# Optimization experiments

Measured on AMD Instinct MI355X. Metric: run time of the kernel, lower is better.

## Reference

```python
import jax, jax.numpy as jnp
import numpy as np

B, S, D = 4, 4096, 1024
H, W = 16, 256
DH = D // H


def setup_inputs() -> dict:
    key = jax.random.key(0)
    ks = jax.random.split(key, 5)
    sc = 1.0 / np.sqrt(D)
    return {
        "x": jax.random.normal(ks[0], (B, S, D), jnp.float32),
        "Wq": jax.random.normal(ks[1], (D, D), jnp.float32) * sc,
        "bq": jnp.zeros((D,), jnp.float32),
        "Wk": jax.random.normal(ks[2], (D, D), jnp.float32) * sc,
        "bk": jnp.zeros((D,), jnp.float32),
        "Wv": jax.random.normal(ks[3], (D, D), jnp.float32) * sc,
        "bv": jnp.zeros((D,), jnp.float32),
        "Wo": jax.random.normal(ks[4], (D, D), jnp.float32) * sc,
        "bo": jnp.zeros((D,), jnp.float32),
    }


def reference(x, Wq, bq, Wk, bk, Wv, bv, Wo, bo):
    b, s, d = x.shape
    n = s // W  # seq divisible by window_size -> no padding

    def split_heads(t):
        # (b, s, d) -> (b, h, n, w, dh)
        return t.reshape(b, n, W, H, DH).transpose(0, 3, 1, 2, 4)

    q = split_heads(x @ Wq + bq)
    k = split_heads(x @ Wk + bk)
    v = split_heads(x @ Wv + bv)

    scores = jnp.einsum("bhnqd,bhnkd->bhnqk", q, k) / jnp.sqrt(
        jnp.asarray(DH, x.dtype)
    )
    causal = jnp.tril(jnp.ones((W, W), bool))  # per-block causal mask
    neg = jnp.finfo(scores.dtype).min
    scores = jnp.where(causal, scores, neg)
    weights = jax.nn.softmax(scores, axis=-1)
    out = jnp.einsum("bhnqk,bhnkd->bhnqd", weights, v)
    # (b, h, n, w, dh) -> (b, s, d)
    out = out.transpose(0, 2, 3, 1, 4).reshape(b, s, d)
    return out @ Wo + bo
```

## Files before the change

kernel.cpp:

```cpp
#include <hip/hip_runtime.h>
#include <hip/hip_bf16.h>


typedef __attribute__((ext_vector_type(4))) float f32x4;
typedef __attribute__((ext_vector_type(8))) short s16x8;
typedef __attribute__((ext_vector_type(4))) short s16x4;

__device__ __forceinline__ short f2bf(float f) {
  unsigned u = __float_as_uint(f);
  u += 0x7fffu + ((u >> 16) & 1u);
  return (short)(u >> 16);
}

__device__ __forceinline__ void gload_lds16(const void* g, void* l) {
  __builtin_amdgcn_global_load_lds((const __attribute__((address_space(1))) void*)g,
                                   (__attribute__((address_space(3))) void*)l,
                                   16, 0, 0);
}

__device__ __forceinline__ float rmax16(float v) {
  v = fmaxf(v, __shfl_xor(v, 1, 64));
  v = fmaxf(v, __shfl_xor(v, 2, 64));
  v = fmaxf(v, __shfl_xor(v, 4, 64));
  v = fmaxf(v, __shfl_xor(v, 8, 64));
  return v;
}
__device__ __forceinline__ float rsum16(float v) {
  v += __shfl_xor(v, 1, 64);
  v += __shfl_xor(v, 2, 64);
  v += __shfl_xor(v, 4, 64);
  v += __shfl_xor(v, 8, 64);
  return v;
}

__global__ void cvt_x(const float4* __restrict__ in, s16x4* __restrict__ out, int n4) {
  for (int i = blockIdx.x * 256 + threadIdx.x; i < n4; i += gridDim.x * 256) {
    float4 v = in[i];
    s16x4 o;
    o[0] = f2bf(v.x); o[1] = f2bf(v.y); o[2] = f2bf(v.z); o[3] = f2bf(v.w);
    out[i] = o;
  }
}

__global__ void cvt_wT(const float* __restrict__ W0, const float* __restrict__ W1,
                       const float* __restrict__ W2, const float* __restrict__ W3,
                       short* __restrict__ out) {
  __shared__ float tile[64][65];
  const float* W = (blockIdx.y == 0) ? W0 : (blockIdx.y == 1) ? W1 : (blockIdx.y == 2) ? W2 : W3;
  short* o = out + (size_t)blockIdx.y * (1024 * 1024);
  const int kt = (blockIdx.x >> 4) << 6, nt = (blockIdx.x & 15) << 6;
  const int tid = threadIdx.x;
#pragma unroll
  for (int i = 0; i < 16; ++i) {
    int lin = i * 256 + tid;
    int r = lin >> 6, c = lin & 63;
    tile[r][c] = W[(size_t)(kt + r) * 1024 + nt + c];
  }
  __syncthreads();
#pragma unroll
  for (int i = 0; i < 16; ++i) {
    int lin = i * 256 + tid;
    int r = lin >> 6, c = lin & 63;
    o[(size_t)(nt + r) * 1024 + kt + c] = f2bf(tile[c][r]);
  }
}

template <int NBN, int MODE>
__global__ __launch_bounds__(512, 2) void gemm8(const short* __restrict__ A,
                                                const short* __restrict__ BtBase,
                                                const float* __restrict__ b0,
                                                const float* __restrict__ b1,
                                                const float* __restrict__ b2,
                                                short* __restrict__ Qo,
                                                short* __restrict__ Ko,
                                                short* __restrict__ Vo,
                                                float* __restrict__ Oo) {
  __shared__ short As[2][16384];
  __shared__ short Bs[2][16384];
  const int tid = threadIdx.x;
  const int wid = tid >> 6, lane = tid & 63;
  const int fr = lane & 15, g = lane >> 4;
  const int wr = wid >> 2, wc = wid & 3;
  const int fswz = (fr & 7) << 4;
  const int d = blockIdx.x;
  const int xcd = d & 7, l = d >> 3;
  const int bm = xcd * 8 + l / NBN, bn = l % NBN;
  const int m0 = bm << 8, n0 = bn << 8;
  const int which = n0 >> 10;
  const char* Ab = (const char*)(A + (size_t)m0 * 1024);
  const char* Bb = (const char*)(BtBase + (size_t)which * 1048576 + (size_t)(n0 & 1023) * 1024);

  const int srow = tid >> 3;
  const int kb = ((tid & 7) << 4) ^ ((srow & 7) << 4);
  const char* aSrc = Ab + (size_t)srow * 2048 + kb;
  const char* bSrc = Bb + (size_t)srow * 2048 + kb;
  const int ldsOff = wid << 10;

#define STAGE2(srcp, dstp, i0, tt)                                            \
  do {                                                                        \
    gload_lds16((srcp) + (size_t)(i0) * 131072 + (size_t)(tt) * 128,          \
                (dstp) + (i0) * 8192 + ldsOff);                               \
    gload_lds16((srcp) + (size_t)((i0) + 1) * 131072 + (size_t)(tt) * 128,    \
                (dstp) + ((i0) + 1) * 8192 + ldsOff);                         \
  } while (0)

#define AFRAG(mi, ks) (*(const s16x8*)(Acur + ((((wr) << 7) + (mi) * 16 + fr) << 7) + \
                                       ((((ks) << 6) | (g << 4)) ^ fswz)))
#define BFRAG(ni, ks) (*(const s16x8*)(Bcur + ((((wc) << 6) + (ni) * 16 + fr) << 7) + \
                                       ((((ks) << 6) | (g << 4)) ^ fswz)))

#define PHASE_MID()                                       \
  __builtin_amdgcn_s_barrier();                           \
  asm volatile("s_waitcnt lgkmcnt(0)" ::: "memory");      \
  __builtin_amdgcn_sched_barrier(0);                      \
  __builtin_amdgcn_s_setprio(1)

#define PHASE_END()                                       \
  __builtin_amdgcn_s_setprio(0);                          \
  __builtin_amdgcn_s_barrier()

  f32x4 acc[8][4];
#pragma unroll
  for (int i = 0; i < 8; ++i)
#pragma unroll
    for (int j = 0; j < 4; ++j) acc[i][j] = (f32x4){0.f, 0.f, 0.f, 0.f};

  {
    char* A0 = (char*)&As[0][0];
    char* B0 = (char*)&Bs[0][0];
    STAGE2(aSrc, A0, 0, 0); STAGE2(aSrc, A0, 2, 0);
    STAGE2(bSrc, B0, 0, 0); STAGE2(bSrc, B0, 2, 0);
  }

#pragma unroll 2
  for (int t = 0; t < 16; ++t) {
    const int cur = t & 1;
    const int tn = t + 1;
    const bool pre = (t < 15);
    const char* Acur = (const char*)&As[cur][0];
    const char* Bcur = (const char*)&Bs[cur][0];
    char* Anxt = (char*)&As[cur ^ 1][0];
    char* Bnxt = (char*)&Bs[cur ^ 1][0];

    asm volatile("s_waitcnt vmcnt(0)" ::: "memory");
    __builtin_amdgcn_s_barrier();

    s16x8 aF[2][4], bF0[2][2], bF1[2][2];
#pragma unroll
    for (int ks = 0; ks < 2; ++ks) {
#pragma unroll
      for (int mi = 0; mi < 4; ++mi) aF[ks][mi] = AFRAG(mi, ks);
#pragma unroll
      for (int ni = 0; ni < 2; ++ni) bF0[ks][ni] = BFRAG(ni, ks);
    }
    if (pre) STAGE2(aSrc, Anxt, 0, tn);
    PHASE_MID();
#pragma unroll
    for (int ks = 0; ks < 2; ++ks)
#pragma unroll
      for (int mi = 0; mi < 4; ++mi)
#pragma unroll
        for (int ni = 0; ni < 2; ++ni)
          acc[mi][ni] = __builtin_amdgcn_mfma_f32_16x16x32_bf16(aF[ks][mi], bF0[ks][ni], acc[mi][ni], 0, 0, 0);
    PHASE_END();

#pragma unroll
    for (int ks = 0; ks < 2; ++ks)
#pragma unroll
      for (int ni = 0; ni < 2; ++ni) bF1[ks][ni] = BFRAG(2 + ni, ks);
    if (pre) STAGE2(aSrc, Anxt, 2, tn);
    PHASE_MID();
#pragma unroll
    for (int ks = 0; ks < 2; ++ks)
#pragma unroll
      for (int mi = 0; mi < 4; ++mi)
#pragma unroll
        for (int ni = 0; ni < 2; ++ni)
          acc[mi][2 + ni] = __builtin_amdgcn_mfma_f32_16x16x32_bf16(aF[ks][mi], bF1[ks][ni], acc[mi][2 + ni], 0, 0, 0);
    PHASE_END();

#pragma unroll
    for (int ks = 0; ks < 2; ++ks)
#pragma unroll
      for (int mi = 0; mi < 4; ++mi) aF[ks][mi] = AFRAG(4 + mi, ks);
    if (pre) STAGE2(bSrc, Bnxt, 0, tn);
    PHASE_MID();
#pragma unroll
    for (int ks = 0; ks < 2; ++ks)
#pragma unroll
      for (int mi = 0; mi < 4; ++mi)
#pragma unroll
        for (int ni = 0; ni < 2; ++ni)
          acc[4 + mi][2 + ni] = __builtin_amdgcn_mfma_f32_16x16x32_bf16(aF[ks][mi], bF1[ks][ni], acc[4 + mi][2 + ni], 0, 0, 0);
    PHASE_END();

    if (pre) STAGE2(bSrc, Bnxt, 2, tn);
    PHASE_MID();
#pragma unroll
    for (int ks = 0; ks < 2; ++ks)
#pragma unroll
      for (int mi = 0; mi < 4; ++mi)
#pragma unroll
        for (int ni = 0; ni < 2; ++ni)
          acc[4 + mi][ni] = __builtin_amdgcn_mfma_f32_16x16x32_bf16(aF[ks][mi], bF0[ks][ni], acc[4 + mi][ni], 0, 0, 0);
    PHASE_END();
  }
#undef STAGE2
#undef AFRAG
#undef BFRAG
#undef PHASE_MID
#undef PHASE_END

  const float* bb = (which == 0) ? b0 : (which == 1) ? b1 : b2;
  const int row0 = m0 + wr * 128 + (g << 2);
  const int col0 = n0 + wc * 64 + fr;
#pragma unroll
  for (int mi = 0; mi < 8; ++mi) {
#pragma unroll
    for (int ni = 0; ni < 4; ++ni) {
      const int c = col0 + ni * 16;
      const float bv = bb[c & 1023];
#pragma unroll
      for (int jj = 0; jj < 4; ++jj) {
        const int r = row0 + mi * 16 + jj;
        const float v = acc[mi][ni][jj] + bv;
        if (MODE == 2) {
          Oo[(size_t)r * 1024 + c] = v;
        } else {
          const int b = r >> 12, s = r & 4095;
          const int cl = c & 1023;
          const int h = cl >> 6, dh = cl & 63;
          short* ob = (which == 0) ? Qo : (which == 1) ? Ko : Vo;
          size_t addr;
          if (which < 2) addr = ((size_t)(b * 16 + h) * 4096 + s) * 64 + dh;
          else           addr = ((size_t)(b * 16 + h) * 64 + dh) * 4096 + s;
          ob[addr] = f2bf(v);
        }
      }
    }
  }
}

__global__ __launch_bounds__(256) void attn_kernel(const short* __restrict__ Qg,
                                                   const short* __restrict__ Kg,
                                                   const short* __restrict__ Vg,
                                                   short* __restrict__ AO) {
  constexpr int S = 4096;
  __shared__ short Pl[4][16][272];
  const int tid = threadIdx.x;
  const int w = tid >> 6, lane = tid & 63;
  const int fr = lane & 15, g = lane >> 4;
  const int idx = blockIdx.x;
  const int qq = idx & 3;
  const int nb = (idx >> 2) & 15, bh = idx >> 6;
  const int b = bh >> 4, h = bh & 15;
  const short* Qb = Qg + ((size_t)bh * S + nb * 256) * 64;
  const short* Kb = Kg + ((size_t)bh * S + nb * 256) * 64;
  const short* Vb = Vg + (size_t)bh * 64 * S + nb * 256;

  const int qrow = qq * 64 + w * 16;
  const int dmax = qq * 4 + w;
  const s16x8 aq0 = *(const s16x8*)&Qb[(qrow + fr) * 64 + (g << 3)];
  const s16x8 aq1 = *(const s16x8*)&Qb[(qrow + fr) * 64 + 32 + (g << 3)];
  f32x4 sc[16];
#pragma unroll
  for (int i = 0; i < 16; ++i) sc[i] = (f32x4){0.f, 0.f, 0.f, 0.f};
#pragma unroll
  for (int kt = 0; kt < 16; ++kt) {
    if (kt <= dmax) {
      const s16x8 kf0 = *(const s16x8*)&Kb[(kt * 16 + fr) * 64 + (g << 3)];
      const s16x8 kf1 = *(const s16x8*)&Kb[(kt * 16 + fr) * 64 + 32 + (g << 3)];
      sc[kt] = __builtin_amdgcn_mfma_f32_16x16x32_bf16(aq0, kf0, sc[kt], 0, 0, 0);
      sc[kt] = __builtin_amdgcn_mfma_f32_16x16x32_bf16(aq1, kf1, sc[kt], 0, 0, 0);
    }
  }
  float mrow[4] = {-3e38f, -3e38f, -3e38f, -3e38f};
#pragma unroll
  for (int kt = 0; kt < 16; ++kt) {
    if (kt <= dmax) {
#pragma unroll
      for (int jj = 0; jj < 4; ++jj) {
        float v = sc[kt][jj] * 0.125f;
        if (kt == dmax && fr > (g << 2) + jj) v = -3e38f;
        sc[kt][jj] = v;
        mrow[jj] = fmaxf(mrow[jj], v);
      }
    }
  }
#pragma unroll
  for (int jj = 0; jj < 4; ++jj) mrow[jj] = rmax16(mrow[jj]);
  float lsum[4] = {0.f, 0.f, 0.f, 0.f};
#pragma unroll
  for (int kt = 0; kt < 16; ++kt) {
    if (kt <= dmax) {
#pragma unroll
      for (int jj = 0; jj < 4; ++jj) {
        const float p = __expf(sc[kt][jj] - mrow[jj]);
        sc[kt][jj] = p;
        lsum[jj] += p;
      }
    }
  }
#pragma unroll
  for (int jj = 0; jj < 4; ++jj) lsum[jj] = rsum16(lsum[jj]);
#pragma unroll
  for (int kt = 0; kt < 16; ++kt) {
    if (kt <= dmax) {
#pragma unroll
      for (int jj = 0; jj < 4; ++jj)
        Pl[w][(g << 2) + jj][kt * 16 + fr] = f2bf(sc[kt][jj]);
    } else if (kt == dmax + 1 && ((dmax + 1) & 1)) {
#pragma unroll
      for (int jj = 0; jj < 4; ++jj) Pl[w][(g << 2) + jj][kt * 16 + fr] = 0;
    }
  }
  asm volatile("s_waitcnt lgkmcnt(0)" ::: "memory");
  f32x4 o[4];
#pragma unroll
  for (int di = 0; di < 4; ++di) o[di] = (f32x4){0.f, 0.f, 0.f, 0.f};
  const int nks2 = (dmax + 2) >> 1;
#pragma unroll
  for (int ks2 = 0; ks2 < 8; ++ks2) {
    if (ks2 < nks2) {
      const s16x8 pa = *(const s16x8*)&Pl[w][fr][ks2 * 32 + (g << 3)];
#pragma unroll
      for (int di = 0; di < 4; ++di) {
        const s16x8 vf = *(const s16x8*)&Vb[(size_t)(di * 16 + fr) * S + ks2 * 32 + (g << 3)];
        o[di] = __builtin_amdgcn_mfma_f32_16x16x32_bf16(pa, vf, o[di], 0, 0, 0);
      }
    }
  }
  float inv[4];
#pragma unroll
  for (int jj = 0; jj < 4; ++jj) inv[jj] = 1.f / lsum[jj];
  const int sg = nb * 256 + qrow + (g << 2);
#pragma unroll
  for (int di = 0; di < 4; ++di) {
#pragma unroll
    for (int jj = 0; jj < 4; ++jj) {
      AO[((size_t)b * S + sg + jj) * 1024 + h * 64 + di * 16 + fr] =
          f2bf(o[di][jj] * inv[jj]);
    }
  }
}

extern "C" void kernel_launch(void* const* d_in, const int* in_sizes, int n_in,
                              void* d_out, int out_size, void* d_ws, size_t ws_size,
                              hipStream_t stream) {
  const float* x  = (const float*)d_in[0];
  const float* Wq = (const float*)d_in[1];
  const float* bq = (const float*)d_in[2];
  const float* Wk = (const float*)d_in[3];
  const float* bk = (const float*)d_in[4];
  const float* Wv = (const float*)d_in[5];
  const float* bv = (const float*)d_in[6];
  const float* Wo = (const float*)d_in[7];
  const float* bo = (const float*)d_in[8];
  float* out = (float*)d_out;

  char* ws = (char*)d_ws;
  short* xb  = (short*)ws;
  short* Wt  = (short*)(ws + (size_t)33554432);
  short* Qb  = (short*)(ws + (size_t)33554432 + 8388608);
  short* Kb  = Qb + (size_t)16777216;
  short* Vb  = Kb + (size_t)16777216;
  short* AOb = Vb + (size_t)16777216;

  cvt_x<<<4096, 256, 0, stream>>>((const float4*)x, (s16x4*)xb, 16777216 / 4);
  cvt_wT<<<dim3(256, 4), 256, 0, stream>>>(Wq, Wk, Wv, Wo, Wt);

  gemm8<12, 0><<<768, 512, 0, stream>>>(xb, Wt, bq, bk, bv, Qb, Kb, Vb, nullptr);

  attn_kernel<<<4096, 256, 0, stream>>>(Qb, Kb, Vb, AOb);

  gemm8<4, 2><<<256, 512, 0, stream>>>(AOb, Wt + 3145728, bo, bo, bo,
                                       nullptr, nullptr, nullptr, out);
}
```

Measured before the change: 481.6 us.

## Restructure GEMM pipeline to prefetch whole next tile, merge attention query blocks

The GEMM main loop now issues all global-to-LDS loads for the next K tile at the top of each iteration. It waits with a partial vmcnt and runs the MFMA work in two larger phases, replacing four barrier-separated phases. This cuts barriers and aims to overlap the next tile's loads with the current compute. The attention kernel now handles a full 256-row window per block, each wave looping over four 16-row query tiles, so the grid shrinks fourfold. Wave workloads become more unbalanced under the causal mask, and the lower block count could reduce latency hiding.

```diff
diff --git a/kernel.cpp b/kernel.cpp
--- a/kernel.cpp
+++ b/kernel.cpp
@@ -66,7 +66,7 @@
 }
 
 template <int NBN, int MODE>
-__global__ __launch_bounds__(512, 2) void gemm8(const short* __restrict__ A,
+__global__ __launch_bounds__(512, 2) void gemm9(const short* __restrict__ A,
                                                 const short* __restrict__ BtBase,
                                                 const float* __restrict__ b0,
                                                 const float* __restrict__ b1,
@@ -96,12 +96,14 @@
   const char* bSrc = Bb + (size_t)srow * 2048 + kb;
   const int ldsOff = wid << 10;
 
-#define STAGE2(srcp, dstp, i0, tt)                                            \
+#define STAGE_ALL(dstA, dstB, tt)                                             \
   do {                                                                        \
-    gload_lds16((srcp) + (size_t)(i0) * 131072 + (size_t)(tt) * 128,          \
-                (dstp) + (i0) * 8192 + ldsOff);                               \
-    gload_lds16((srcp) + (size_t)((i0) + 1) * 131072 + (size_t)(tt) * 128,    \
-                (dstp) + ((i0) + 1) * 8192 + ldsOff);                         \
+    _Pragma("unroll") for (int i = 0; i < 4; ++i)                             \
+      gload_lds16(aSrc + (size_t)i * 131072 + (size_t)(tt) * 128,             \
+                  (dstA) + i * 8192 + ldsOff);                                \
+    _Pragma("unroll") for (int i = 0; i < 4; ++i)                             \
+      gload_lds16(bSrc + (size_t)i * 131072 + (size_t)(tt) * 128,             \
+                  (dstB) + i * 8192 + ldsOff);                                \
   } while (0)
 
 #define AFRAG(mi, ks) (*(const s16x8*)(Acur + ((((wr) << 7) + (mi) * 16 + fr) << 7) + \
@@ -109,41 +111,27 @@
 #define BFRAG(ni, ks) (*(const s16x8*)(Bcur + ((((wc) << 6) + (ni) * 16 + fr) << 7) + \
                                        ((((ks) << 6) | (g << 4)) ^ fswz)))
 
-#define PHASE_MID()                                       \
-  __builtin_amdgcn_s_barrier();                           \
-  asm volatile("s_waitcnt lgkmcnt(0)" ::: "memory");      \
-  __builtin_amdgcn_sched_barrier(0);                      \
-  __builtin_amdgcn_s_setprio(1)
-
-#define PHASE_END()                                       \
-  __builtin_amdgcn_s_setprio(0);                          \
-  __builtin_amdgcn_s_barrier()
-
   f32x4 acc[8][4];
 #pragma unroll
   for (int i = 0; i < 8; ++i)
 #pragma unroll
     for (int j = 0; j < 4; ++j) acc[i][j] = (f32x4){0.f, 0.f, 0.f, 0.f};
 
-  {
-    char* A0 = (char*)&As[0][0];
-    char* B0 = (char*)&Bs[0][0];
-    STAGE2(aSrc, A0, 0, 0); STAGE2(aSrc, A0, 2, 0);
-    STAGE2(bSrc, B0, 0, 0); STAGE2(bSrc, B0, 2, 0);
-  }
+  STAGE_ALL((char*)&As[0][0], (char*)&Bs[0][0], 0);
 
 #pragma unroll 2
   for (int t = 0; t < 16; ++t) {
     const int cur = t & 1;
-    const int tn = t + 1;
-    const bool pre = (t < 15);
     const char* Acur = (const char*)&As[cur][0];
     const char* Bcur = (const char*)&Bs[cur][0];
-    char* Anxt = (char*)&As[cur ^ 1][0];
-    char* Bnxt = (char*)&Bs[cur ^ 1][0];
-
-    asm volatile("s_waitcnt vmcnt(0)" ::: "memory");
+
+    if (t < 15) STAGE_ALL((char*)&As[cur ^ 1][0], (char*)&Bs[cur ^ 1][0], t + 1);
+
+    if (t < 15) asm volatile("s_waitcnt vmcnt(8)" ::: "memory");
+    else        asm volatile("s_waitcnt vmcnt(0)" ::: "memory");
+    __builtin_amdgcn_sched_barrier(0);
     __builtin_amdgcn_s_barrier();
+    __builtin_amdgcn_s_setprio(1);
 
     s16x8 aF[2][4], bF0[2][2], bF1[2][2];
 #pragma unroll
@@ -151,65 +139,40 @@
 #pragma unroll
       for (int mi = 0; mi < 4; ++mi) aF[ks][mi] = AFRAG(mi, ks);
 #pragma unroll
-      for (int ni = 0; ni < 2; ++ni) bF0[ks][ni] = BFRAG(ni, ks);
-    }
-    if (pre) STAGE2(aSrc, Anxt, 0, tn);
-    PHASE_MID();
+      for (int ni = 0; ni < 2; ++ni) { bF0[ks][ni] = BFRAG(ni, ks); bF1[ks][ni] = BFRAG(2 + ni, ks); }
+    }
 #pragma unroll
     for (int ks = 0; ks < 2; ++ks)
 #pragma unroll
       for (int mi = 0; mi < 4; ++mi)
 #pragma unroll
-        for (int ni = 0; ni < 2; ++ni)
-          acc[mi][ni] = __builtin_amdgcn_mfma_f32_16x16x32_bf16(aF[ks][mi], bF0[ks][ni], acc[mi][ni], 0, 0, 0);
-    PHASE_END();
+        for (int ni = 0; ni < 2; ++ni) {
+          acc[mi][ni]     = __builtin_amdgcn_mfma_f32_16x16x32_bf16(aF[ks][mi], bF0[ks][ni], acc[mi][ni], 0, 0, 0);
+          acc[mi][2 + ni] = __builtin_amdgcn_mfma_f32_16x16x32_bf16(aF[ks][mi], bF1[ks][ni], acc[mi][2 + ni], 0, 0, 0);
+        }
 
 #pragma unroll
     for (int ks = 0; ks < 2; ++ks)
 #pragma unroll
-      for (int ni = 0; ni < 2; ++ni) bF1[ks][ni] = BFRAG(2 + ni, ks);
-    if (pre) STAGE2(aSrc, Anxt, 2, tn);
-    PHASE_MID();
+      for (int mi = 0; mi < 4; ++mi) aF[ks][mi] = AFRAG(4 + mi, ks);
 #pragma unroll
     for (int ks = 0; ks < 2; ++ks)
 #pragma unroll
       for (int mi = 0; mi < 4; ++mi)
 #pragma unroll
-        for (int ni = 0; ni < 2; ++ni)
-          acc[mi][2 + ni] = __builtin_amdgcn_mfma_f32_16x16x32_bf16(aF[ks][mi], bF1[ks][ni], acc[mi][2 + ni], 0, 0, 0);
-    PHASE_END();
-
-#pragma unroll
-    for (int ks = 0; ks < 2; ++ks)
-#pragma unroll
-      for (int mi = 0; mi < 4; ++mi) aF[ks][mi] = AFRAG(4 + mi, ks);
-    if (pre) STAGE2(bSrc, Bnxt, 0, tn);
-    PHASE_MID();
-#pragma unroll
-    for (int ks = 0; ks < 2; ++ks)
-#pragma unroll
-      for (int mi = 0; mi < 4; ++mi)
-#pragma unroll
-        for (int ni = 0; ni < 2; ++ni)
+        for (int ni = 0; ni < 2; ++ni) {
+          acc[4 + mi][ni]     = __builtin_amdgcn_mfma_f32_16x16x32_bf16(aF[ks][mi], bF0[ks][ni], acc[4 + mi][ni], 0, 0, 0);
           acc[4 + mi][2 + ni] = __builtin_amdgcn_mfma_f32_16x16x32_bf16(aF[ks][mi], bF1[ks][ni], acc[4 + mi][2 + ni], 0, 0, 0);
-    PHASE_END();
-
-    if (pre) STAGE2(bSrc, Bnxt, 2, tn);
-    PHASE_MID();
-#pragma unroll
-    for (int ks = 0; ks < 2; ++ks)
-#pragma unroll
-      for (int mi = 0; mi < 4; ++mi)
-#pragma unroll
-        for (int ni = 0; ni < 2; ++ni)
-          acc[4 + mi][ni] = __builtin_amdgcn_mfma_f32_16x16x32_bf16(aF[ks][mi], bF0[ks][ni], acc[4 + mi][ni], 0, 0, 0);
-    PHASE_END();
-  }
-#undef STAGE2
+        }
+
+    __builtin_amdgcn_s_setprio(0);
+    asm volatile("s_waitcnt lgkmcnt(0)" ::: "memory");
+    __builtin_amdgcn_sched_barrier(0);
+    __builtin_amdgcn_s_barrier();
+  }
+#undef STAGE_ALL
 #undef AFRAG
 #undef BFRAG
-#undef PHASE_MID
-#undef PHASE_END
 
   const float* bb = (which == 0) ? b0 : (which == 1) ? b1 : b2;
   const int row0 = m0 + wr * 128 + (g << 2);
@@ -250,96 +213,98 @@
   const int tid = threadIdx.x;
   const int w = tid >> 6, lane = tid & 63;
   const int fr = lane & 15, g = lane >> 4;
-  const int idx = blockIdx.x;
-  const int qq = idx & 3;
-  const int nb = (idx >> 2) & 15, bh = idx >> 6;
+  const int bhn = blockIdx.x;
+  const int nb = bhn & 15, bh = bhn >> 4;
   const int b = bh >> 4, h = bh & 15;
   const short* Qb = Qg + ((size_t)bh * S + nb * 256) * 64;
   const short* Kb = Kg + ((size_t)bh * S + nb * 256) * 64;
   const short* Vb = Vg + (size_t)bh * 64 * S + nb * 256;
 
-  const int qrow = qq * 64 + w * 16;
-  const int dmax = qq * 4 + w;
-  const s16x8 aq0 = *(const s16x8*)&Qb[(qrow + fr) * 64 + (g << 3)];
-  const s16x8 aq1 = *(const s16x8*)&Qb[(qrow + fr) * 64 + 32 + (g << 3)];
-  f32x4 sc[16];
-#pragma unroll
-  for (int i = 0; i < 16; ++i) sc[i] = (f32x4){0.f, 0.f, 0.f, 0.f};
-#pragma unroll
-  for (int kt = 0; kt < 16; ++kt) {
-    if (kt <= dmax) {
-      const s16x8 kf0 = *(const s16x8*)&Kb[(kt * 16 + fr) * 64 + (g << 3)];
-      const s16x8 kf1 = *(const s16x8*)&Kb[(kt * 16 + fr) * 64 + 32 + (g << 3)];
-      sc[kt] = __builtin_amdgcn_mfma_f32_16x16x32_bf16(aq0, kf0, sc[kt], 0, 0, 0);
-      sc[kt] = __builtin_amdgcn_mfma_f32_16x16x32_bf16(aq1, kf1, sc[kt], 0, 0, 0);
-    }
-  }
-  float mrow[4] = {-3e38f, -3e38f, -3e38f, -3e38f};
-#pragma unroll
-  for (int kt = 0; kt < 16; ++kt) {
-    if (kt <= dmax) {
+#pragma unroll
+  for (int qi = 0; qi < 4; ++qi) {
+    const int qrow = w * 64 + qi * 16;
+    const int dmax = w * 4 + qi;
+    const s16x8 aq0 = *(const s16x8*)&Qb[(qrow + fr) * 64 + (g << 3)];
+    const s16x8 aq1 = *(const s16x8*)&Qb[(qrow + fr) * 64 + 32 + (g << 3)];
+    f32x4 sc[16];
+#pragma unroll
+    for (int i = 0; i < 16; ++i) sc[i] = (f32x4){0.f, 0.f, 0.f, 0.f};
+#pragma unroll
+    for (int kt = 0; kt < 16; ++kt) {
+      if (kt <= dmax) {
+        const s16x8 kf0 = *(const s16x8*)&Kb[(kt * 16 + fr) * 64 + (g << 3)];
+        const s16x8 kf1 = *(const s16x8*)&Kb[(kt * 16 + fr) * 64 + 32 + (g << 3)];
+        sc[kt] = __builtin_amdgcn_mfma_f32_16x16x32_bf16(aq0, kf0, sc[kt], 0, 0, 0);
+        sc[kt] = __builtin_amdgcn_mfma_f32_16x16x32_bf16(aq1, kf1, sc[kt], 0, 0, 0);
+      }
+    }
+    float mrow[4] = {-3e38f, -3e38f, -3e38f, -3e38f};
+#pragma unroll
+    for (int kt = 0; kt < 16; ++kt) {
+      if (kt <= dmax) {
+#pragma unroll
+        for (int jj = 0; jj < 4; ++jj) {
+          float v = sc[kt][jj] * 0.125f;
+          if (kt == dmax && fr > (g << 2) + jj) v = -3e38f;
+          sc[kt][jj] = v;
+          mrow[jj] = fmaxf(mrow[jj], v);
+        }
+      }
+    }
+#pragma unroll
+    for (int jj = 0; jj < 4; ++jj) mrow[jj] = rmax16(mrow[jj]);
+    float lsum[4] = {0.f, 0.f, 0.f, 0.f};
+#pragma unroll
+    for (int kt = 0; kt < 16; ++kt) {
+      if (kt <= dmax) {
+#pragma unroll
+        for (int jj = 0; jj < 4; ++jj) {
+          const float p = __expf(sc[kt][jj] - mrow[jj]);
+          sc[kt][jj] = p;
+          lsum[jj] += p;
+        }
+      }
+    }
+#pragma unroll
+    for (int jj = 0; jj < 4; ++jj) lsum[jj] = rsum16(lsum[jj]);
+#pragma unroll
+    for (int kt = 0; kt < 16; ++kt) {
+      if (kt <= dmax) {
+#pragma unroll
+        for (int jj = 0; jj < 4; ++jj)
+          Pl[w][(g << 2) + jj][kt * 16 + fr] = f2bf(sc[kt][jj]);
+      } else if (kt == dmax + 1 && ((dmax + 1) & 1)) {
+#pragma unroll
+        for (int jj = 0; jj < 4; ++jj) Pl[w][(g << 2) + jj][kt * 16 + fr] = 0;
+      }
+    }
+    asm volatile("s_waitcnt lgkmcnt(0)" ::: "memory");
+    f32x4 o[4];
+#pragma unroll
+    for (int di = 0; di < 4; ++di) o[di] = (f32x4){0.f, 0.f, 0.f, 0.f};
+    const int nks2 = (dmax + 2) >> 1;
+#pragma unroll
+    for (int ks2 = 0; ks2 < 8; ++ks2) {
+      if (ks2 < nks2) {
+        const s16x8 pa = *(const s16x8*)&Pl[w][fr][ks2 * 32 + (g << 3)];
+#pragma unroll
+        for (int di = 0; di < 4; ++di) {
+          const s16x8 vf = *(const s16x8*)&Vb[(size_t)(di * 16 + fr) * S + ks2 * 32 + (g << 3)];
+          o[di] = __builtin_amdgcn_mfma_f32_16x16x32_bf16(pa, vf, o[di], 0, 0, 0);
+        }
+      }
+    }
+    float inv[4];
+#pragma unroll
+    for (int jj = 0; jj < 4; ++jj) inv[jj] = 1.f / lsum[jj];
+    const int sg = nb * 256 + qrow + (g << 2);
+#pragma unroll
+    for (int di = 0; di < 4; ++di) {
 #pragma unroll
       for (int jj = 0; jj < 4; ++jj) {
-        float v = sc[kt][jj] * 0.125f;
-        if (kt == dmax && fr > (g << 2) + jj) v = -3e38f;
-        sc[kt][jj] = v;
-        mrow[jj] = fmaxf(mrow[jj], v);
-      }
-    }
-  }
-#pragma unroll
-  for (int jj = 0; jj < 4; ++jj) mrow[jj] = rmax16(mrow[jj]);
-  float lsum[4] = {0.f, 0.f, 0.f, 0.f};
-#pragma unroll
-  for (int kt = 0; kt < 16; ++kt) {
-    if (kt <= dmax) {
-#pragma unroll
-      for (int jj = 0; jj < 4; ++jj) {
-        const float p = __expf(sc[kt][jj] - mrow[jj]);
-        sc[kt][jj] = p;
-        lsum[jj] += p;
-      }
-    }
-  }
-#pragma unroll
-  for (int jj = 0; jj < 4; ++jj) lsum[jj] = rsum16(lsum[jj]);
-#pragma unroll
-  for (int kt = 0; kt < 16; ++kt) {
-    if (kt <= dmax) {
-#pragma unroll
-      for (int jj = 0; jj < 4; ++jj)
-        Pl[w][(g << 2) + jj][kt * 16 + fr] = f2bf(sc[kt][jj]);
-    } else if (kt == dmax + 1 && ((dmax + 1) & 1)) {
-#pragma unroll
-      for (int jj = 0; jj < 4; ++jj) Pl[w][(g << 2) + jj][kt * 16 + fr] = 0;
-    }
-  }
-  asm volatile("s_waitcnt lgkmcnt(0)" ::: "memory");
-  f32x4 o[4];
-#pragma unroll
-  for (int di = 0; di < 4; ++di) o[di] = (f32x4){0.f, 0.f, 0.f, 0.f};
-  const int nks2 = (dmax + 2) >> 1;
-#pragma unroll
-  for (int ks2 = 0; ks2 < 8; ++ks2) {
-    if (ks2 < nks2) {
-      const s16x8 pa = *(const s16x8*)&Pl[w][fr][ks2 * 32 + (g << 3)];
-#pragma unroll
-      for (int di = 0; di < 4; ++di) {
-        const s16x8 vf = *(const s16x8*)&Vb[(size_t)(di * 16 + fr) * S + ks2 * 32 + (g << 3)];
-        o[di] = __builtin_amdgcn_mfma_f32_16x16x32_bf16(pa, vf, o[di], 0, 0, 0);
-      }
-    }
-  }
-  float inv[4];
-#pragma unroll
-  for (int jj = 0; jj < 4; ++jj) inv[jj] = 1.f / lsum[jj];
-  const int sg = nb * 256 + qrow + (g << 2);
-#pragma unroll
-  for (int di = 0; di < 4; ++di) {
-#pragma unroll
-    for (int jj = 0; jj < 4; ++jj) {
-      AO[((size_t)b * S + sg + jj) * 1024 + h * 64 + di * 16 + fr] =
-          f2bf(o[di][jj] * inv[jj]);
+        AO[((size_t)b * S + sg + jj) * 1024 + h * 64 + di * 16 + fr] =
+            f2bf(o[di][jj] * inv[jj]);
+      }
     }
   }
 }
@@ -369,10 +334,10 @@
   cvt_x<<<4096, 256, 0, stream>>>((const float4*)x, (s16x4*)xb, 16777216 / 4);
   cvt_wT<<<dim3(256, 4), 256, 0, stream>>>(Wq, Wk, Wv, Wo, Wt);
 
-  gemm8<12, 0><<<768, 512, 0, stream>>>(xb, Wt, bq, bk, bv, Qb, Kb, Vb, nullptr);
-
-  attn_kernel<<<4096, 256, 0, stream>>>(Qb, Kb, Vb, AOb);
-
-  gemm8<4, 2><<<256, 512, 0, stream>>>(AOb, Wt + 3145728, bo, bo, bo,
+  gemm9<12, 0><<<768, 512, 0, stream>>>(xb, Wt, bq, bk, bv, Qb, Kb, Vb, nullptr);
+
+  attn_kernel<<<1024, 256, 0, stream>>>(Qb, Kb, Vb, AOb);
+
+  gemm9<4, 2><<<256, 512, 0, stream>>>(AOb, Wt + 3145728, bo, bo, bo,
                                        nullptr, nullptr, nullptr, out);
 }
```

Result: faster. 426.0 us (-11.5%).
